# Optimization experiments

Hardware: AMD Instinct MI355X
Metric: run time of the kernel (lower is better)

## Reference

```python
import jax, jax.numpy as jnp
import numpy as np

VERTS = [5023, 1256, 314, 79, 20]
SPIRAL_LEN = 9
T_FRAMES = 32
LATENT = 64


def _spiral_conv(x, idx, W, b):
    # x: [B, N, C]; idx: [N, L]; gather spiral neighborhoods then linear
    B = x.shape[0]
    g = x[:, idx.reshape(-1), :].reshape(B, idx.shape[0], -1)  # [B, N, L*C]
    return g @ W.T + b


def _pool(x, rows, cols, vals, n_out):
    # sparse matmul: out[b, rows] += x[b, cols] * vals  (index_select + scatter_add)
    gathered = x[:, cols, :] * vals[None, :, None]
    return jnp.zeros((x.shape[0], n_out, x.shape[2]), x.dtype).at[:, rows, :].add(gathered)


def _lstm_dir(x, Wih, Whh, bih, bhh, reverse):
    # x: [T, B, D]; PyTorch gate order i, f, g, o
    Bz, H = x.shape[1], Whh.shape[1]
    bias = bih + bhh
    def step(carry, xt):
        h, c = carry
        g = xt @ Wih.T + h @ Whh.T + bias
        i, f, gg, o = jnp.split(g, 4, axis=-1)
        c = jax.nn.sigmoid(f) * c + jax.nn.sigmoid(i) * jnp.tanh(gg)
        h = jax.nn.sigmoid(o) * jnp.tanh(c)
        return (h, c), h
    init = (jnp.zeros((Bz, H), x.dtype), jnp.zeros((Bz, H), x.dtype))
    _, hs = jax.lax.scan(step, init, x, reverse=reverse)
    return hs


def _forward(audio_hidden, vertices, actor,
             sp_idx0, sp_idx1, sp_idx2, sp_idx3,
             d0_rows, d0_cols, d0_vals, d1_rows, d1_cols, d1_vals,
             d2_rows, d2_cols, d2_vals, d3_rows, d3_cols, d3_vals,
             u0_rows, u0_cols, u0_vals, u1_rows, u1_cols, u1_vals,
             u2_rows, u2_cols, u2_vals, u3_rows, u3_cols, u3_vals,
             enc_W0, enc_b0, enc_W1, enc_b1, enc_W2, enc_b2, enc_W3, enc_b3,
             enc_lin_W, enc_lin_b, dec_lin_W, dec_lin_b,
             dec_W0, dec_b0, dec_W1, dec_b1, dec_W2, dec_b2, dec_W3, dec_b3,
             dec_W4, dec_b4, aud_W, aud_b,
             l0_Wih, l0_Whh, l0_bih, l0_bhh, l12_Wih, l12_Whh, l12_bih, l12_bhh):
    ah = audio_hidden
    if ah.shape[1] % 2 != 0:
        ah = ah[:, :ah.shape[1] - 1]
    tv = vertices.shape[1]
    if ah.shape[1] > 2 * tv:
        ah = ah[:, :2 * tv]
    elif ah.shape[1] < 2 * tv:
        tv = ah.shape[1] // 2
    hs = ah.reshape(1, ah.shape[1] // 2, ah.shape[2] * 2)[:, :tv]  # [1, T, 1536]
    audio_emb = hs @ aud_W.T + aud_b                                # [1, T, LATENT]
    # --- mesh encoder on actor template: (spiral conv -> ELU -> down pool) x4 -> Linear ---
    sp = (sp_idx0, sp_idx1, sp_idx2, sp_idx3)
    down = ((d0_rows, d0_cols, d0_vals), (d1_rows, d1_cols, d1_vals),
            (d2_rows, d2_cols, d2_vals), (d3_rows, d3_cols, d3_vals))
    encp = ((enc_W0, enc_b0), (enc_W1, enc_b1), (enc_W2, enc_b2), (enc_W3, enc_b3))
    x = actor
    for i in range(4):
        x = jax.nn.elu(_spiral_conv(x, sp[i], *encp[i]))
        x = _pool(x, *down[i], VERTS[i + 1])
    z = x.reshape(x.shape[0], -1) @ enc_lin_W.T + enc_lin_b        # [1, LATENT]
    actor_emb = jnp.broadcast_to(z[:, None, :], audio_emb.shape)
    # --- 3-layer bidirectional LSTM ---
    h = jnp.concatenate([audio_emb, actor_emb], axis=-1).transpose(1, 0, 2)  # [T, 1, 2*LATENT]
    for layer in range(3):
        if layer == 0:
            Wih, Whh, bih, bhh = l0_Wih, l0_Whh, l0_bih, l0_bhh
        else:
            Wih, Whh, bih, bhh = l12_Wih[layer - 1], l12_Whh[layer - 1], l12_bih[layer - 1], l12_bhh[layer - 1]
        f = _lstm_dir(h, Wih[0], Whh[0], bih[0], bhh[0], False)
        r = _lstm_dir(h, Wih[1], Whh[1], bih[1], bhh[1], True)
        h = jnp.concatenate([f, r], axis=-1)
    latent = h.transpose(1, 0, 2)[0]                               # [T, LATENT]
    # --- mesh decoder, batched over all frames (replaces the python per-frame loop) ---
    up = ((u0_rows, u0_cols, u0_vals), (u1_rows, u1_cols, u1_vals),
          (u2_rows, u2_cols, u2_vals), (u3_rows, u3_cols, u3_vals))
    decp = ((dec_W0, dec_b0), (dec_W1, dec_b1), (dec_W2, dec_b2), (dec_W3, dec_b3))
    y = latent @ dec_lin_W.T + dec_lin_b                           # [T, 20*256]
    y = y.reshape(y.shape[0], VERTS[4], -1)                        # [T, 20, 256]
    for i in range(4):
        j = 3 - i
        y = _pool(y, *up[j], VERTS[j])
        y = jax.nn.elu(_spiral_conv(y, sp[j], *decp[i]))
    y = _spiral_conv(y, sp[0], dec_W4, dec_b4)                     # [T, 5023, 3]
    return y + actor                                               # broadcast residual, == vstacked preds


def setup_inputs() -> dict:
    key = jax.random.key(0)
    ks = iter(jax.random.split(key, 96))
    def nrm(shape, s=0.05):
        return jax.random.normal(next(ks), shape, jnp.float32) * s
    def rint(shape, hi):
        return jax.random.randint(next(ks), shape, 0, hi)
    inp = {}
    inp['audio_hidden'] = nrm((1, 2 * T_FRAMES, 768), 1.0)
    inp['vertices'] = nrm((1, T_FRAMES, VERTS[0], 3), 1.0)
    inp['actor'] = nrm((1, VERTS[0], 3), 1.0)
    for i in range(4):
        inp['sp_idx%d' % i] = rint((VERTS[i], SPIRAL_LEN), VERTS[i])
    for i in range(4):
        nnz = 3 * VERTS[i + 1]
        inp['d%d_rows' % i] = rint((nnz,), VERTS[i + 1])
        inp['d%d_cols' % i] = rint((nnz,), VERTS[i])
        inp['d%d_vals' % i] = jax.random.uniform(next(ks), (nnz,), jnp.float32)
    for i in range(4):
        nnz = 3 * VERTS[i]
        inp['u%d_rows' % i] = rint((nnz,), VERTS[i])
        inp['u%d_cols' % i] = rint((nnz,), VERTS[i + 1])
        inp['u%d_vals' % i] = jax.random.uniform(next(ks), (nnz,), jnp.float32)
    OC = [32, 64, 128, 256]
    ic = 3
    for i in range(4):
        inp['enc_W%d' % i] = nrm((OC[i], ic * SPIRAL_LEN))
        inp['enc_b%d' % i] = nrm((OC[i],))
        ic = OC[i]
    inp['enc_lin_W'] = nrm((LATENT, VERTS[4] * OC[3]))
    inp['enc_lin_b'] = nrm((LATENT,))
    inp['dec_lin_W'] = nrm((VERTS[4] * OC[3], LATENT))
    inp['dec_lin_b'] = nrm((VERTS[4] * OC[3],))
    dic = [256, 256, 128, 64]
    doc = [256, 128, 64, 32]
    for i in range(4):
        inp['dec_W%d' % i] = nrm((doc[i], dic[i] * SPIRAL_LEN))
        inp['dec_b%d' % i] = nrm((doc[i],))
    inp['dec_W4'] = nrm((3, OC[0] * SPIRAL_LEN))
    inp['dec_b4'] = nrm((3,))
    inp['aud_W'] = nrm((LATENT, 1536))
    inp['aud_b'] = nrm((LATENT,))
    H = LATENT // 2
    inp['l0_Wih'] = nrm((2, 4 * H, 2 * LATENT))
    inp['l0_Whh'] = nrm((2, 4 * H, H))
    inp['l0_bih'] = nrm((2, 4 * H))
    inp['l0_bhh'] = nrm((2, 4 * H))
    inp['l12_Wih'] = nrm((2, 2, 4 * H, 2 * H))
    inp['l12_Whh'] = nrm((2, 2, 4 * H, H))
    inp['l12_bih'] = nrm((2, 2, 4 * H))
    inp['l12_bhh'] = nrm((2, 2, 4 * H))
    return inp


def reference(audio_hidden, vertices, actor,
              sp_idx0, sp_idx1, sp_idx2, sp_idx3,
              d0_rows, d0_cols, d0_vals, d1_rows, d1_cols, d1_vals,
              d2_rows, d2_cols, d2_vals, d3_rows, d3_cols, d3_vals,
              u0_rows, u0_cols, u0_vals, u1_rows, u1_cols, u1_vals,
              u2_rows, u2_cols, u2_vals, u3_rows, u3_cols, u3_vals,
              enc_W0, enc_b0, enc_W1, enc_b1, enc_W2, enc_b2, enc_W3, enc_b3,
              enc_lin_W, enc_lin_b, dec_lin_W, dec_lin_b,
              dec_W0, dec_b0, dec_W1, dec_b1, dec_W2, dec_b2, dec_W3, dec_b3,
              dec_W4, dec_b4, aud_W, aud_b,
              l0_Wih, l0_Whh, l0_bih, l0_bhh, l12_Wih, l12_Whh, l12_bih, l12_bhh):
    return _forward(audio_hidden, vertices, actor,
                    sp_idx0, sp_idx1, sp_idx2, sp_idx3,
                    d0_rows, d0_cols, d0_vals, d1_rows, d1_cols, d1_vals,
                    d2_rows, d2_cols, d2_vals, d3_rows, d3_cols, d3_vals,
                    u0_rows, u0_cols, u0_vals, u1_rows, u1_cols, u1_vals,
                    u2_rows, u2_cols, u2_vals, u3_rows, u3_cols, u3_vals,
                    enc_W0, enc_b0, enc_W1, enc_b1, enc_W2, enc_b2, enc_W3, enc_b3,
                    enc_lin_W, enc_lin_b, dec_lin_W, dec_lin_b,
                    dec_W0, dec_b0, dec_W1, dec_b1, dec_W2, dec_b2, dec_W3, dec_b3,
                    dec_W4, dec_b4, aud_W, aud_b,
                    l0_Wih, l0_Whh, l0_bih, l0_bhh, l12_Wih, l12_Whh, l12_bih, l12_bhh)
```

## Files before the change

### kernel.cpp

```cpp
#include <hip/hip_runtime.h>
#include <cstdint>
#include <cstddef>


typedef unsigned short u16;
typedef __attribute__((ext_vector_type(8))) short short8;
typedef __attribute__((ext_vector_type(4))) float float4v;
#define CDIV(a,b) (((a)+(b)-1)/(b))
#define POOL_CAP 64

__device__ __forceinline__ float bf(u16 u){ return __uint_as_float(((unsigned)u)<<16); }
__device__ __forceinline__ u16 fb(float x){
  unsigned u = __float_as_uint(x);
  unsigned r = u + 0x7fffu + ((u>>16)&1u);
  return (u16)(r>>16);
}
__device__ __forceinline__ float lo16(unsigned u){ return __uint_as_float(u<<16); }
__device__ __forceinline__ float hi16(unsigned u){ return __uint_as_float(u & 0xffff0000u); }

struct WCast { const float* src[7]; int cum[8]; };
__global__ void cast_all_k(WCast C, u16* __restrict__ dst, int total){
  int i = blockIdx.x*blockDim.x + threadIdx.x;
  if (i >= total) return;
  int k = 0;
  while (i >= C.cum[k+1]) k++;
  dst[i] = fb(C.src[k][i - C.cum[k]]);
}

__global__ void audio_emb_k(const float* __restrict__ ah, const float* __restrict__ W,
                            const float* __restrict__ b, float* __restrict__ h0){
  int t = blockIdx.x;
  int f = threadIdx.x >> 2, sl = threadIdx.x & 3;
  const float4* x4 = (const float4*)(ah + t*1536);
  const float4* w4 = (const float4*)(W + f*1536);
  float acc = 0.f;
  for (int k=sl; k<384; k+=4){
    float4 xv = x4[k], wv = w4[k];
    acc += xv.x*wv.x + xv.y*wv.y + xv.z*wv.z + xv.w*wv.w;
  }
  acc += __shfl_down(acc, 2, 64);
  acc += __shfl_down(acc, 1, 64);
  if (sl == 0) h0[t*128 + f] = acc + b[f];
}

__global__ void conv3_k(const float* __restrict__ x, const int* __restrict__ idx,
                        const float* __restrict__ W, const float* __restrict__ bias,
                        u16* __restrict__ out, int V, int OC){
  int i = blockIdx.x*blockDim.x + threadIdx.x;
  if (i >= V*OC) return;
  int o = i % OC; int v = i / OC;
  const float* wrow = W + (size_t)o*27;
  const int* vix = idx + v*9;
  float acc = bias[o];
  for (int s=0;s<9;s++){
    const float* xr = x + (size_t)vix[s]*3;
    acc += xr[0]*wrow[s*3] + xr[1]*wrow[s*3+1] + xr[2]*wrow[s*3+2];
  }
  if (acc < 0.f) acc = expm1f(acc);
  out[i] = fb(acc);
}

template<int IC, int BN, int BM>
__global__ void __launch_bounds__(256) conv_mfma(
    const u16* __restrict__ x, const int* __restrict__ idx,
    const u16* __restrict__ Wb, const float* __restrict__ bias,
    u16* __restrict__ out, int V, int OC, int M){
  constexpr int K = 9*IC;
  constexpr int NT = BN/16;
  constexpr int MT = BM/64;
  constexpr int LOG2 = (IC==32?5: IC==64?6: IC==128?7:8);
  constexpr int AST = 40;
  __shared__ u16 Asm[BM*AST];
  __shared__ u16 Bsm[BN*AST];
  __shared__ int rowB[BM], rowV[BM];
  int t = threadIdx.x;
  int m0 = blockIdx.x*BM;
  int o0 = blockIdx.y*BN;
  if (t < BM){
    int mg = m0 + t;
    if (mg < M){ int b = mg / V; rowB[t] = b; rowV[t] = mg - b*V; }
    else rowB[t] = -1;
  }
  int lane = t & 63, wave = t >> 6;
  int quad = lane >> 4, col = lane & 15;
  float4v acc[MT][NT];
  #pragma unroll
  for (int mi=0;mi<MT;mi++)
    #pragma unroll
    for (int nt=0;nt<NT;nt++) acc[mi][nt] = (float4v)0.f;

  for (int kc = 0; kc < K/32; ++kc){
    int s  = (kc*32) >> LOG2;
    int c0 = (kc*32) & (IC-1);
    __syncthreads();
    #pragma unroll
    for (int rpt=0; rpt<MT; ++rpt){
      int seg = t + 256*rpt;
      int arow = seg >> 2, aq = seg & 3;
      int b = rowB[arow];
      uint4 val = {0u,0u,0u,0u};
      if (b >= 0){
        int ix = idx[rowV[arow]*9 + s];
        val = *(const uint4*)(x + ((size_t)b*V + ix)*IC + c0 + aq*8);
      }
      *(uint4*)&Asm[arow*AST + aq*8] = val;
    }
    if (t < BN*4){
      int br = t >> 2, bq = t & 3;
      *(uint4*)&Bsm[br*AST + bq*8] =
          *(const uint4*)(Wb + (size_t)(o0+br)*K + kc*32 + bq*8);
    }
    __syncthreads();
    short8 a[MT];
    #pragma unroll
    for (int mi=0;mi<MT;mi++)
      a[mi] = *(const short8*)&Asm[(wave*MT*16 + mi*16 + col)*AST + quad*8];
    #pragma unroll
    for (int nt=0; nt<NT; ++nt){
      short8 bfr = *(const short8*)&Bsm[(nt*16 + col)*AST + quad*8];
      #pragma unroll
      for (int mi=0;mi<MT;mi++)
        acc[mi][nt] = __builtin_amdgcn_mfma_f32_16x16x32_bf16(a[mi], bfr, acc[mi][nt], 0, 0, 0);
    }
  }
  #pragma unroll
  for (int mi=0;mi<MT;mi++){
    #pragma unroll
    for (int nt=0; nt<NT; ++nt){
      int o = o0 + nt*16 + col;
      float bv = bias[o];
      #pragma unroll
      for (int r=0;r<4;r++){
        int mg = m0 + wave*MT*16 + mi*16 + quad*4 + r;
        if (mg < M){
          float val = acc[mi][nt][r] + bv;
          if (val < 0.f) val = expm1f(val);
          out[(size_t)mg*OC + o] = fb(val);
        }
      }
    }
  }
}

struct Lists {
  const int* rows[8];
  int nnz[8];
  int curoff[8];
  int lstoff[8];
};
__global__ void fill_all_k(Lists L, int* __restrict__ curBase, int* __restrict__ lstBase, int total){
  int i = blockIdx.x*blockDim.x + threadIdx.x;
  if (i >= total) return;
  int off = i, k = 0;
  while (off >= L.nnz[k]){ off -= L.nnz[k]; k++; }
  int r = L.rows[k][off];
  int p = atomicAdd(curBase + L.curoff[k] + r, 1);
  if (p < POOL_CAP) lstBase[L.lstoff[k] + r*POOL_CAP + p] = off;
}

__global__ void pool_g4_k(const u16* __restrict__ x, const int* __restrict__ cols,
                          const float* __restrict__ vals, const int* __restrict__ cur,
                          const int* __restrict__ lst, u16* __restrict__ out,
                          int B, int Vin, int Vout, int C){
  int C4 = C >> 2;
  int total = B*Vout*C4;
  int i = blockIdx.x*blockDim.x + threadIdx.x;
  if (i >= total) return;
  int c4 = i % C4; int tt = i / C4; int r = tt % Vout; int b = tt / Vout;
  int deg = cur[r]; if (deg > POOL_CAP) deg = POOL_CAP;
  const int* le = lst + r*POOL_CAP;
  float a0=0.f,a1=0.f,a2=0.f,a3=0.f;
  for (int k=0;k<deg;k++){
    int e = le[k];
    float v = vals[e];
    ushort4 xv = *(const ushort4*)(x + ((size_t)b*Vin + (size_t)cols[e])*C + c4*4);
    a0 += v*bf(xv.x); a1 += v*bf(xv.y); a2 += v*bf(xv.z); a3 += v*bf(xv.w);
  }
  ushort4 o; o.x=fb(a0); o.y=fb(a1); o.z=fb(a2); o.w=fb(a3);
  *(ushort4*)(out + ((size_t)b*Vout + (size_t)r)*C + c4*4) = o;
}

__global__ void __launch_bounds__(256) enc_lin_k(
    const u16* __restrict__ x, const float* __restrict__ W,
    const float* __restrict__ b, float* __restrict__ h0){
  int f = blockIdx.x;
  int t = threadIdx.x;
  const ushort4* x4 = (const ushort4*)x;
  const float4* w4 = (const float4*)(W + (size_t)f*5120);
  float acc = 0.f;
  for (int k=t; k<1280; k+=256){
    ushort4 xv = x4[k]; float4 wv = w4[k];
    acc += bf(xv.x)*wv.x + bf(xv.y)*wv.y + bf(xv.z)*wv.z + bf(xv.w)*wv.w;
  }
  #pragma unroll
  for (int off=32; off; off>>=1) acc += __shfl_down(acc, off, 64);
  __shared__ float red[4];
  if ((t & 63) == 0) red[t>>6] = acc;
  __syncthreads();
  if (t < 32){
    float zf = b[f] + red[0] + red[1] + red[2] + red[3];
    h0[t*128 + 64 + f] = zf;
  }
}

__device__ __forceinline__ float sigm(float x){ return 1.f/(1.f+__expf(-x)); }
__device__ __forceinline__ float tanhfast(float x){ return 1.f - 2.f/(__expf(2.f*x)+1.f); }

__global__ void __launch_bounds__(256) lstm3_k(
    const float* __restrict__ h0,
    const float* __restrict__ l0_Wih, const float* __restrict__ l0_Whh,
    const float* __restrict__ l0_bih, const float* __restrict__ l0_bhh,
    const float* __restrict__ l12_Wih, const float* __restrict__ l12_Whh,
    const float* __restrict__ l12_bih, const float* __restrict__ l12_bhh,
    float* __restrict__ latent){
  __shared__ __align__(16) u16 xb[32*136];
  __shared__ __align__(16) float xp[2*32*128];
  __shared__ __align__(16) u16 obuf[32*64];
  __shared__ __align__(16) u16 hsh[2][32];
  __shared__ float bias_l[256];
  int t = threadIdx.x;
  int lane = t & 63, wave = t >> 6;
  int quad = lane >> 4, col = lane & 15;
  int dir = t >> 7;
  bool rev = (dir == 1);
  int w2 = (t >> 6) & 1;
  int unit = w2*16 + col;
  int jj = quad*32 + unit;

  for (int i=t;i<32*128;i+=256){ int tt=i>>7, k=i&127; xb[tt*136+k]=fb(h0[i]); }

  for (int layer=0; layer<3; layer++){
    int IN = (layer==0)?128:64;
    const float *Wih,*Whh,*bih,*bhh;
    if (layer==0){ Wih=l0_Wih; Whh=l0_Whh; bih=l0_bih; bhh=l0_bhh; }
    else {
      int mb=(layer-1)*2;
      Wih=l12_Wih + (size_t)mb*128*64; Whh=l12_Whh + (size_t)mb*128*32;
      bih=l12_bih + mb*128; bhh=l12_bhh + mb*128;
    }
    const float* WhhD = Whh + (size_t)dir*128*32 + (size_t)jj*32;
    unsigned whh[16];
    #pragma unroll
    for (int k=0;k<16;k++){
      float2 w = *(const float2*)&WhhD[2*k];
      whh[k] = ((unsigned)fb(w.x)) | (((unsigned)fb(w.y))<<16);
    }
    bias_l[t] = bih[dir*128 + (t&127)] + bhh[dir*128 + (t&127)];
    if (quad == 0) hsh[dir][unit] = 0;
    float creg = 0.f;
    __syncthreads();

    {
      int dirA = wave >> 1, o0 = (wave & 1)*64;
      const float* WA = Wih + (size_t)dirA*128*IN;
      float4v acc[2][4];
      #pragma unroll
      for (int mi=0;mi<2;mi++)
        #pragma unroll
        for (int nt=0;nt<4;nt++) acc[mi][nt] = (float4v)0.f;
      for (int kc=0; kc<IN/32; ++kc){
        short8 bfrag[4];
        #pragma unroll
        for (int nt=0;nt<4;nt++){
          const float* src = WA + (size_t)(o0+nt*16+col)*IN + kc*32 + quad*8;
          float4 w0 = *(const float4*)src;
          float4 w1 = *(const float4*)(src+4);
          alignas(16) u16 tmp[8] = {fb(w0.x),fb(w0.y),fb(w0.z),fb(w0.w),
                                    fb(w1.x),fb(w1.y),fb(w1.z),fb(w1.w)};
          bfrag[nt] = *(const short8*)tmp;
        }
        short8 afrag[2];
        #pragma unroll
        for (int mi=0;mi<2;mi++)
          afrag[mi] = *(const short8*)&xb[(mi*16+col)*136 + kc*32 + quad*8];
        #pragma unroll
        for (int nt=0;nt<4;nt++)
          #pragma unroll
          for (int mi=0;mi<2;mi++)
            acc[mi][nt] = __builtin_amdgcn_mfma_f32_16x16x32_bf16(afrag[mi], bfrag[nt], acc[mi][nt], 0, 0, 0);
      }
      #pragma unroll
      for (int mi=0;mi<2;mi++)
        #pragma unroll
        for (int nt=0;nt<4;nt++){
          int j = o0 + nt*16 + col;
          float bv = bias_l[dirA*128 + j];
          #pragma unroll
          for (int r=0;r<4;r++){
            int tt = mi*16 + quad*4 + r;
            xp[dirA*4096 + tt*128 + j] = acc[mi][nt][r] + bv;
          }
        }
    }
    __syncthreads();

    for (int s=0;s<32;s++){
      int tx = rev ? (31-s) : s;
      float g = xp[dir*4096 + tx*128 + jj];
      const uint4* h4 = (const uint4*)hsh[dir];
      float a0=0.f,a1=0.f,a2=0.f,a3=0.f;
      #pragma unroll
      for (int k=0;k<4;k++){
        uint4 hv = h4[k];
        unsigned u0=whh[4*k], u1=whh[4*k+1], u2=whh[4*k+2], u3=whh[4*k+3];
        a0 = fmaf(lo16(hv.x), lo16(u0), a0);
        a0 = fmaf(hi16(hv.x), hi16(u0), a0);
        a1 = fmaf(lo16(hv.y), lo16(u1), a1);
        a1 = fmaf(hi16(hv.y), hi16(u1), a1);
        a2 = fmaf(lo16(hv.z), lo16(u2), a2);
        a2 = fmaf(hi16(hv.z), hi16(u2), a2);
        a3 = fmaf(lo16(hv.w), lo16(u3), a3);
        a3 = fmaf(hi16(hv.w), hi16(u3), a3);
      }
      g += (a0+a1) + (a2+a3);
      float act = (quad == 2) ? tanhfast(g) : sigm(g);
      float gi = __shfl(act, col, 64);
      float gf = __shfl(act, 16+col, 64);
      float gg = __shfl(act, 32+col, 64);
      float go = __shfl(act, 48+col, 64);
      if (quad == 0){
        float cn = gf*creg + gi*gg;
        float hn = go*tanhfast(cn);
        creg = cn;
        u16 hb = fb(hn);
        hsh[dir][unit] = hb;
        obuf[tx*64 + dir*32 + unit] = hb;
      }
      __syncthreads();
    }
    if (layer < 2){
      for (int i=t;i<32*64;i+=256){ int tt=i>>6, k=i&63; xb[tt*136+k]=obuf[i]; }
      __syncthreads();
    }
  }
  for (int i=t;i<32*64;i+=256) latent[i] = bf(obuf[i]);
}

__global__ void dec_lin_k(const float* __restrict__ latent, const float* __restrict__ W,
                          const float* __restrict__ b, u16* __restrict__ y){
  int i = blockIdx.x*blockDim.x + threadIdx.x;
  if (i >= 32*5120) return;
  int r = i % 5120, t = i / 5120;
  const float4* x4 = (const float4*)(latent + t*64);
  const float4* w4 = (const float4*)(W + (size_t)r*64);
  float acc = b[r];
  #pragma unroll
  for (int k=0;k<16;k++){
    float4 xv=x4[k]; float4 wv=w4[k];
    acc += xv.x*wv.x+xv.y*wv.y+xv.z*wv.z+xv.w*wv.w;
  }
  y[i] = fb(acc);
}

__global__ void final_k(const u16* __restrict__ x, const int* __restrict__ idx,
                        const float* __restrict__ W, const float* __restrict__ bias,
                        const float* __restrict__ actor, float* __restrict__ out){
  __shared__ float Wsm[3*288];
  __shared__ float bsm[3];
  int t = threadIdx.x;
  for (int i=t;i<864;i+=256) Wsm[i]=W[i];
  if (t<3) bsm[t]=bias[t];
  __syncthreads();
  int g = blockIdx.x*256 + t;
  if (g >= 32*5023) return;
  int v = g % 5023, b = g / 5023;
  const u16* xb = x + (size_t)b*5023*32;
  const int* vix = idx + v*9;
  float a0=bsm[0], a1=bsm[1], a2=bsm[2];
  for (int s=0;s<9;s++){
    const ushort4* xr = (const ushort4*)(xb + (size_t)vix[s]*32);
    #pragma unroll
    for (int k=0;k<8;k++){
      ushort4 xv = xr[k];
      float x0=bf(xv.x), x1=bf(xv.y), x2=bf(xv.z), x3=bf(xv.w);
      int kk = s*32 + k*4;
      a0 += x0*Wsm[kk] + x1*Wsm[kk+1] + x2*Wsm[kk+2] + x3*Wsm[kk+3];
      a1 += x0*Wsm[288+kk] + x1*Wsm[288+kk+1] + x2*Wsm[288+kk+2] + x3*Wsm[288+kk+3];
      a2 += x0*Wsm[576+kk] + x1*Wsm[576+kk+1] + x2*Wsm[576+kk+2] + x3*Wsm[576+kk+3];
    }
  }
  out[(size_t)g*3+0] = a0 + actor[v*3+0];
  out[(size_t)g*3+1] = a1 + actor[v*3+1];
  out[(size_t)g*3+2] = a2 + actor[v*3+2];
}

extern "C" void kernel_launch(void* const* d_in, const int* in_sizes, int n_in,
                              void* d_out, int out_size, void* d_ws, size_t ws_size,
                              hipStream_t stream){
  (void)in_sizes; (void)n_in; (void)out_size; (void)ws_size;

  const float* audio = (const float*)d_in[0];
  const float* actor = (const float*)d_in[2];
  const int* sp[4]   = {(const int*)d_in[3],(const int*)d_in[4],(const int*)d_in[5],(const int*)d_in[6]};
  const int* drows[4]; const int* dcols[4]; const float* dvals[4];
  for (int i=0;i<4;i++){ drows[i]=(const int*)d_in[7+3*i]; dcols[i]=(const int*)d_in[8+3*i]; dvals[i]=(const float*)d_in[9+3*i]; }
  const int* urows[4]; const int* ucols[4]; const float* uvals[4];
  for (int i=0;i<4;i++){ urows[i]=(const int*)d_in[19+3*i]; ucols[i]=(const int*)d_in[20+3*i]; uvals[i]=(const float*)d_in[21+3*i]; }
  const float* encW[4]={(const float*)d_in[31],(const float*)d_in[33],(const float*)d_in[35],(const float*)d_in[37]};
  const float* encB[4]={(const float*)d_in[32],(const float*)d_in[34],(const float*)d_in[36],(const float*)d_in[38]};
  const float* enc_lin_W=(const float*)d_in[39]; const float* enc_lin_b=(const float*)d_in[40];
  const float* dec_lin_W=(const float*)d_in[41]; const float* dec_lin_b=(const float*)d_in[42];
  const float* decW[5]={(const float*)d_in[43],(const float*)d_in[45],(const float*)d_in[47],(const float*)d_in[49],(const float*)d_in[51]};
  const float* decB[5]={(const float*)d_in[44],(const float*)d_in[46],(const float*)d_in[48],(const float*)d_in[50],(const float*)d_in[52]};
  const float* audW=(const float*)d_in[53]; const float* audB=(const float*)d_in[54];
  const float* l0_Wih=(const float*)d_in[55]; const float* l0_Whh=(const float*)d_in[56];
  const float* l0_bih=(const float*)d_in[57]; const float* l0_bhh=(const float*)d_in[58];
  const float* l12_Wih=(const float*)d_in[59]; const float* l12_Whh=(const float*)d_in[60];
  const float* l12_bih=(const float*)d_in[61]; const float* l12_bhh=(const float*)d_in[62];
  float* out = (float*)d_out;

  char* base = (char*)d_ws;
  u16* A  = (u16*)base;
  u16* Bb = (u16*)(base + 10287104);
  int* curBase = (int*)(base + 30891520);
  int* lstBase = (int*)(base + 30924928);
  u16* Wbf = (u16*)(base + 33060224);
  float* sm = (float*)(base + 35788160);
  float* h0     = sm;
  float* latent = sm + 4096;

  const int wsz[7] = {64*288, 128*576, 256*1152, 256*2304, 128*2304, 64*1152, 32*576};
  WCast WC; int wcum = 0;
  const float* wsrc[7] = {encW[1],encW[2],encW[3],decW[0],decW[1],decW[2],decW[3]};
  int wo[7];
  for (int k=0;k<7;k++){ WC.src[k]=wsrc[k]; WC.cum[k]=wcum; wo[k]=wcum; wcum+=wsz[k]; }
  WC.cum[7]=wcum;
  cast_all_k<<<CDIV(wcum,256),256,0,stream>>>(WC, Wbf, wcum);

  const int pVout[8] = {1256,314,79,20,5023,1256,314,79};
  const int pNnz[8]  = {3768,942,237,60,15069,3768,942,237};
  Lists L; int curoff=0, lstoff=0, totnnz=0;
  const int* prow[8] = {drows[0],drows[1],drows[2],drows[3],urows[0],urows[1],urows[2],urows[3]};
  int curo[8], lsto[8];
  for (int k=0;k<8;k++){
    L.rows[k]=prow[k]; L.nnz[k]=pNnz[k];
    L.curoff[k]=curoff; L.lstoff[k]=lstoff;
    curo[k]=curoff; lsto[k]=lstoff;
    curoff += pVout[k]; lstoff += pVout[k]*POOL_CAP; totnnz += pNnz[k];
  }
  hipMemsetAsync(curBase, 0, (size_t)curoff*4, stream);
  fill_all_k<<<CDIV(totnnz,256),256,0,stream>>>(L, curBase, lstBase, totnnz);

  audio_emb_k<<<32,256,0,stream>>>(audio, audW, audB, h0);

  conv3_k<<<CDIV(5023*32,256),256,0,stream>>>(actor, sp[0], encW[0], encB[0], A, 5023, 32);
  pool_g4_k<<<CDIV(1256*8,256),256,0,stream>>>(A, dcols[0], dvals[0], curBase+curo[0], lstBase+lsto[0], Bb, 1, 5023, 1256, 32);
  conv_mfma<32,64,64><<<dim3(CDIV(1256,64),1),256,0,stream>>>(Bb, sp[1], Wbf+wo[0], encB[1], A, 1256, 64, 1256);
  pool_g4_k<<<CDIV(314*16,256),256,0,stream>>>(A, dcols[1], dvals[1], curBase+curo[1], lstBase+lsto[1], Bb, 1, 1256, 314, 64);
  conv_mfma<64,64,64><<<dim3(CDIV(314,64),2),256,0,stream>>>(Bb, sp[2], Wbf+wo[1], encB[2], A, 314, 128, 314);
  pool_g4_k<<<CDIV(79*32,256),256,0,stream>>>(A, dcols[2], dvals[2], curBase+curo[2], lstBase+lsto[2], Bb, 1, 314, 79, 128);
  conv_mfma<128,64,64><<<dim3(CDIV(79,64),4),256,0,stream>>>(Bb, sp[3], Wbf+wo[2], encB[3], A, 79, 256, 79);
  pool_g4_k<<<CDIV(20*64,256),256,0,stream>>>(A, dcols[3], dvals[3], curBase+curo[3], lstBase+lsto[3], Bb, 1, 79, 20, 256);

  enc_lin_k<<<64,256,0,stream>>>(Bb, enc_lin_W, enc_lin_b, h0);

  lstm3_k<<<1,256,0,stream>>>(h0, l0_Wih, l0_Whh, l0_bih, l0_bhh,
                              l12_Wih, l12_Whh, l12_bih, l12_bhh, latent);

  dec_lin_k<<<CDIV(32*5120,256),256,0,stream>>>(latent, dec_lin_W, dec_lin_b, A);

  pool_g4_k<<<CDIV(32*79*64,256),256,0,stream>>>(A, ucols[3], uvals[3], curBase+curo[7], lstBase+lsto[7], Bb, 32, 20, 79, 256);
  conv_mfma<256,64,64><<<dim3(CDIV(2528,64),4),256,0,stream>>>(Bb, sp[3], Wbf+wo[3], decB[0], A, 79, 256, 2528);

  pool_g4_k<<<CDIV(32*314*64,256),256,0,stream>>>(A, ucols[2], uvals[2], curBase+curo[6], lstBase+lsto[6], Bb, 32, 79, 314, 256);
  conv_mfma<256,64,128><<<dim3(CDIV(10048,128),2),256,0,stream>>>(Bb, sp[2], Wbf+wo[4], decB[1], A, 314, 128, 10048);

  pool_g4_k<<<CDIV(32*1256*32,256),256,0,stream>>>(A, ucols[1], uvals[1], curBase+curo[5], lstBase+lsto[5], Bb, 32, 314, 1256, 128);
  conv_mfma<128,64,128><<<dim3(CDIV(40192,128),1),256,0,stream>>>(Bb, sp[1], Wbf+wo[5], decB[2], A, 1256, 64, 40192);

  pool_g4_k<<<CDIV(32*5023*16,256),256,0,stream>>>(A, ucols[0], uvals[0], curBase+curo[4], lstBase+lsto[4], Bb, 32, 1256, 5023, 64);
  conv_mfma<64,32,128><<<dim3(CDIV(160736,128),1),256,0,stream>>>(Bb, sp[0], Wbf+wo[6], decB[3], A, 5023, 32, 160736);

  final_k<<<CDIV(32*5023,256),256,0,stream>>>(A, sp[0], decW[4], decB[4], actor, out);
}
```

Before: 698.1 us.

## Double-buffer conv_mfma LDS tiles with register prefetch and cache spiral indices

The spiral-conv MFMA kernel now keeps two LDS buffers and prefetches the next K-chunk's gathered activations and weights into registers while the current chunk runs through MFMA. This cuts the barriers per iteration from two to one. The spiral neighbour indices for the block's rows are loaded once into shared memory instead of being re-read from global memory on every chunk. One decoder conv launch also drops from BM=128 to BM=64 tiles to get more blocks. The cost is more LDS and registers per block, which may lower occupancy.

```diff
diff --git a/kernel.cpp b/kernel.cpp
--- a/kernel.cpp
+++ b/kernel.cpp
@@ -66,13 +66,15 @@
     const u16* __restrict__ Wb, const float* __restrict__ bias,
     u16* __restrict__ out, int V, int OC, int M){
   constexpr int K = 9*IC;
+  constexpr int KC = K/32;
   constexpr int NT = BN/16;
   constexpr int MT = BM/64;
   constexpr int LOG2 = (IC==32?5: IC==64?6: IC==128?7:8);
   constexpr int AST = 40;
-  __shared__ u16 Asm[BM*AST];
-  __shared__ u16 Bsm[BN*AST];
+  __shared__ u16 Asm[2][BM*AST];
+  __shared__ u16 Bsm[2][BN*AST];
   __shared__ int rowB[BM], rowV[BM];
+  __shared__ int sidx[BM*9];
   int t = threadIdx.x;
   int m0 = blockIdx.x*BM;
   int o0 = blockIdx.y*BN;
@@ -81,6 +83,11 @@
     if (mg < M){ int b = mg / V; rowB[t] = b; rowV[t] = mg - b*V; }
     else rowB[t] = -1;
   }
+  __syncthreads();
+  for (int i=t; i<BM*9; i+=256){
+    int r = i/9, s = i - r*9;
+    sidx[i] = (rowB[r] >= 0) ? idx[rowV[r]*9 + s] : 0;
+  }
   int lane = t & 63, wave = t >> 6;
   int quad = lane >> 4, col = lane & 15;
   float4v acc[MT][NT];
@@ -89,35 +96,52 @@
     #pragma unroll
     for (int nt=0;nt<NT;nt++) acc[mi][nt] = (float4v)0.f;
 
-  for (int kc = 0; kc < K/32; ++kc){
+  uint4 aval[MT]; uint4 bval;
+  auto fetch = [&](int kc){
     int s  = (kc*32) >> LOG2;
     int c0 = (kc*32) & (IC-1);
-    __syncthreads();
     #pragma unroll
     for (int rpt=0; rpt<MT; ++rpt){
       int seg = t + 256*rpt;
       int arow = seg >> 2, aq = seg & 3;
       int b = rowB[arow];
-      uint4 val = {0u,0u,0u,0u};
+      uint4 v = {0u,0u,0u,0u};
       if (b >= 0){
-        int ix = idx[rowV[arow]*9 + s];
-        val = *(const uint4*)(x + ((size_t)b*V + ix)*IC + c0 + aq*8);
+        int ix = sidx[arow*9 + s];
+        v = *(const uint4*)(x + ((size_t)b*V + ix)*IC + c0 + aq*8);
       }
-      *(uint4*)&Asm[arow*AST + aq*8] = val;
+      aval[rpt] = v;
     }
     if (t < BN*4){
       int br = t >> 2, bq = t & 3;
-      *(uint4*)&Bsm[br*AST + bq*8] =
-          *(const uint4*)(Wb + (size_t)(o0+br)*K + kc*32 + bq*8);
+      bval = *(const uint4*)(Wb + (size_t)(o0+br)*K + kc*32 + bq*8);
+    }
+  };
+
+  __syncthreads();
+  fetch(0);
+
+  for (int kc = 0; kc < KC; ++kc){
+    int buf = kc & 1;
+    #pragma unroll
+    for (int rpt=0; rpt<MT; ++rpt){
+      int seg = t + 256*rpt;
+      int arow = seg >> 2, aq = seg & 3;
+      *(uint4*)&Asm[buf][arow*AST + aq*8] = aval[rpt];
+    }
+    if (t < BN*4){
+      int br = t >> 2, bq = t & 3;
+      *(uint4*)&Bsm[buf][br*AST + bq*8] = bval;
     }
     __syncthreads();
+    if (kc+1 < KC) fetch(kc+1);
     short8 a[MT];
     #pragma unroll
     for (int mi=0;mi<MT;mi++)
-      a[mi] = *(const short8*)&Asm[(wave*MT*16 + mi*16 + col)*AST + quad*8];
+      a[mi] = *(const short8*)&Asm[buf][(wave*MT*16 + mi*16 + col)*AST + quad*8];
     #pragma unroll
     for (int nt=0; nt<NT; ++nt){
-      short8 bfr = *(const short8*)&Bsm[(nt*16 + col)*AST + quad*8];
+      short8 bfr = *(const short8*)&Bsm[buf][(nt*16 + col)*AST + quad*8];
       #pragma unroll
       for (int mi=0;mi<MT;mi++)
         acc[mi][nt] = __builtin_amdgcn_mfma_f32_16x16x32_bf16(a[mi], bfr, acc[mi][nt], 0, 0, 0);
@@ -463,7 +487,7 @@
   conv_mfma<256,64,64><<<dim3(CDIV(2528,64),4),256,0,stream>>>(Bb, sp[3], Wbf+wo[3], decB[0], A, 79, 256, 2528);
 
   pool_g4_k<<<CDIV(32*314*64,256),256,0,stream>>>(A, ucols[2], uvals[2], curBase+curo[6], lstBase+lsto[6], Bb, 32, 79, 314, 256);
-  conv_mfma<256,64,128><<<dim3(CDIV(10048,128),2),256,0,stream>>>(Bb, sp[2], Wbf+wo[4], decB[1], A, 314, 128, 10048);
+  conv_mfma<256,64,64><<<dim3(CDIV(10048,64),2),256,0,stream>>>(Bb, sp[2], Wbf+wo[4], decB[1], A, 314, 128, 10048);
 
   pool_g4_k<<<CDIV(32*1256*32,256),256,0,stream>>>(A, ucols[1], uvals[1], curBase+curo[5], lstBase+lsto[5], Bb, 32, 314, 1256, 128);
   conv_mfma<128,64,128><<<dim3(CDIV(40192,128),1),256,0,stream>>>(Bb, sp[1], Wbf+wo[5], decB[2], A, 1256, 64, 40192);
```

Result: faster. 591.0 us (-15.3%).
